# Kernel tuning notes

Hardware: AMD Instinct MI355X
Metric: run time of the kernel (lower is better)

The kernel has to match this reference:

```python
import jax, jax.numpy as jnp
import numpy as np

EMBED_DIM = 1024
NUM_HEADS = 16
HEAD_DIM = EMBED_DIM // NUM_HEADS


def setup_inputs() -> dict:
    key = jax.random.key(0)
    ks = jax.random.split(key, 5)
    x = jax.random.normal(ks[0], (2, 2048, EMBED_DIM), dtype=jnp.float32)
    s_in = 1.0 / np.sqrt(EMBED_DIM)
    W_qkv = jax.random.uniform(ks[1], (EMBED_DIM, 3 * EMBED_DIM), minval=-s_in, maxval=s_in, dtype=jnp.float32)
    b_qkv = jax.random.uniform(ks[2], (3 * EMBED_DIM,), minval=-s_in, maxval=s_in, dtype=jnp.float32)
    W_out = jax.random.uniform(ks[3], (EMBED_DIM, EMBED_DIM), minval=-s_in, maxval=s_in, dtype=jnp.float32)
    b_out = jax.random.uniform(ks[4], (EMBED_DIM,), minval=-s_in, maxval=s_in, dtype=jnp.float32)
    return {"x": x, "W_qkv": W_qkv, "b_qkv": b_qkv, "W_out": W_out, "b_out": b_out}


def reference(x, W_qkv, b_qkv, W_out, b_out):
    B, S, D = x.shape
    H, Dh = NUM_HEADS, HEAD_DIM
    qkv = x @ W_qkv + b_qkv                       # [B, S, 3D]
    q, k, v = jnp.split(qkv, 3, axis=-1)
    # [B, S, D] -> [B, H, S, Dh]
    q = q.reshape(B, S, H, Dh).transpose(0, 2, 1, 3)
    k = k.reshape(B, S, H, Dh).transpose(0, 2, 1, 3)
    v = v.reshape(B, S, H, Dh).transpose(0, 2, 1, 3)
    scores = jnp.einsum('bhqd,bhkd->bhqk', q, k) / jnp.sqrt(jnp.float32(Dh))
    probs = jax.nn.softmax(scores, axis=-1)       # [B, H, S, S]
    attn = jnp.einsum('bhqk,bhkd->bhqd', probs, v)
    attn = attn.transpose(0, 2, 1, 3).reshape(B, S, D)
    return attn @ W_out + b_out
```

## Files before the change

### kernel.cpp

```cpp
#include <hip/hip_runtime.h>
#include <hip/hip_bf16.h>

#define DEV __device__ __forceinline__

typedef __bf16 bf16x8 __attribute__((ext_vector_type(8)));
typedef float f32x4 __attribute__((ext_vector_type(4)));
typedef float f32x16 __attribute__((ext_vector_type(16)));
using u16 = unsigned short;
using u32 = unsigned int;

static constexpr int S = 2048;
static constexpr int D = 1024;
static constexpr float SCQ = 0.125f * 1.44269504088896340736f;

DEV u16 f2bf(float f) {
  unsigned u = __builtin_bit_cast(unsigned, f);
  u += 0x7fffu + ((u >> 16) & 1u);
  return (u16)(u >> 16);
}
DEV u32 pk2(float a, float b) {
  u32 ua = __builtin_bit_cast(u32, a) + 0x8000u;
  u32 ub = __builtin_bit_cast(u32, b) + 0x8000u;
  return __builtin_amdgcn_perm(ub, ua, 0x07060302);
}

__global__ void k_pack(const float* __restrict__ in, u16* __restrict__ out, int n4) {
  int i = blockIdx.x * blockDim.x + threadIdx.x;
  if (i < n4) {
    const float4 v = reinterpret_cast<const float4*>(in)[i];
    ushort4 o;
    o.x = f2bf(v.x); o.y = f2bf(v.y); o.z = f2bf(v.z); o.w = f2bf(v.w);
    reinterpret_cast<ushort4*>(out)[i] = o;
  }
}

__global__ void k_transpose(const float* __restrict__ in, u16* __restrict__ out, int R, int C) {
  __shared__ float t[32][33];
  int c0 = blockIdx.x * 32, r0 = blockIdx.y * 32;
  for (int i = threadIdx.y; i < 32; i += 8)
    t[i][threadIdx.x] = in[(size_t)(r0 + i) * C + c0 + threadIdx.x];
  __syncthreads();
  for (int i = threadIdx.y; i < 32; i += 8)
    out[(size_t)(c0 + i) * R + r0 + threadIdx.x] = f2bf(t[threadIdx.x][i]);
}

template <int MODE>
__global__ __launch_bounds__(256) void k_gemm(const u16* __restrict__ A, const u16* __restrict__ Bt,
                                              const float* __restrict__ bias, int M, int N, int K,
                                              u16* __restrict__ Qb, u16* __restrict__ Kb,
                                              u16* __restrict__ Vt, float* __restrict__ outF) {
  __shared__ u16 As[128][40];
  __shared__ u16 Bs[128][40];
  const int tid = threadIdx.x;
  const int lane = tid & 63, wave = tid >> 6;
  const int l15 = lane & 15, quad = lane >> 4;
  const int m0 = blockIdx.y * 128, n0 = blockIdx.x * 128;
  const int wm = (wave >> 1) * 64, wn = (wave & 1) * 64;
  const int row0 = tid >> 2, c0 = (tid & 3) * 8;
  const int row1 = (tid + 256) >> 2, c1 = (tid & 3) * 8;

  f32x4 acc[4][4];
#pragma unroll
  for (int i = 0; i < 4; i++)
#pragma unroll
    for (int j = 0; j < 4; j++) acc[i][j] = (f32x4){0.f, 0.f, 0.f, 0.f};

  uint4 pa0 = *reinterpret_cast<const uint4*>(&A[(size_t)(m0 + row0) * K + c0]);
  uint4 pa1 = *reinterpret_cast<const uint4*>(&A[(size_t)(m0 + row1) * K + c1]);
  uint4 pb0 = *reinterpret_cast<const uint4*>(&Bt[(size_t)(n0 + row0) * K + c0]);
  uint4 pb1 = *reinterpret_cast<const uint4*>(&Bt[(size_t)(n0 + row1) * K + c1]);

  for (int kk = 0; kk < K; kk += 32) {
    __syncthreads();
    *reinterpret_cast<uint4*>(&As[row0][c0]) = pa0;
    *reinterpret_cast<uint4*>(&As[row1][c1]) = pa1;
    *reinterpret_cast<uint4*>(&Bs[row0][c0]) = pb0;
    *reinterpret_cast<uint4*>(&Bs[row1][c1]) = pb1;
    __syncthreads();
    if (kk + 32 < K) {
      pa0 = *reinterpret_cast<const uint4*>(&A[(size_t)(m0 + row0) * K + kk + 32 + c0]);
      pa1 = *reinterpret_cast<const uint4*>(&A[(size_t)(m0 + row1) * K + kk + 32 + c1]);
      pb0 = *reinterpret_cast<const uint4*>(&Bt[(size_t)(n0 + row0) * K + kk + 32 + c0]);
      pb1 = *reinterpret_cast<const uint4*>(&Bt[(size_t)(n0 + row1) * K + kk + 32 + c1]);
    }
    bf16x8 af[4], bfv[4];
#pragma unroll
    for (int i = 0; i < 4; i++) {
      af[i] = *reinterpret_cast<const bf16x8*>(&As[wm + i * 16 + l15][quad * 8]);
      bfv[i] = *reinterpret_cast<const bf16x8*>(&Bs[wn + i * 16 + l15][quad * 8]);
    }
#pragma unroll
    for (int i = 0; i < 4; i++)
#pragma unroll
      for (int j = 0; j < 4; j++)
        acc[i][j] = __builtin_amdgcn_mfma_f32_16x16x32_bf16(af[i], bfv[j], acc[i][j], 0, 0, 0);
  }

#pragma unroll
  for (int i = 0; i < 4; i++) {
#pragma unroll
    for (int j = 0; j < 4; j++) {
#pragma unroll
      for (int r = 0; r < 4; r++) {
        int m = m0 + wm + i * 16 + quad * 4 + r;
        int n = n0 + wn + j * 16 + l15;
        float v = acc[i][j][r] + bias[n];
        if (MODE == 0) {
          int which = n >> 10;
          int h = (n >> 6) & 15, dh = n & 63;
          int b = m >> 11, s = m & 2047;
          int bh = b * 16 + h;
          if (which == 0)      Qb[((size_t)bh * S + s) * 64 + dh] = f2bf(v * SCQ);
          else if (which == 1) Kb[((size_t)bh * S + s) * 64 + dh] = f2bf(v);
          else                 Vt[((size_t)bh * 64 + dh) * S + s] = f2bf(v);
        } else {
          outF[(size_t)m * N + n] = v;
        }
      }
    }
  }
}

__global__ __launch_bounds__(256, 2) void k_attn(const u16* __restrict__ Qb,
                                                 const u16* __restrict__ Kb,
                                                 const u16* __restrict__ Vt,
                                                 u16* __restrict__ attnB) {
  __shared__ u16 Ks[64][72];
  __shared__ u16 Vs[64][72];
  __shared__ u16 Pl[4][32][72];
  const int bh = blockIdx.y;
  const int q0 = blockIdx.x * 128;
  const int tid = threadIdx.x;
  const int lane = tid & 63, wave = tid >> 6;
  const int l31 = lane & 31, hi = lane >> 5;
  const u16* Qh = Qb + (size_t)bh * S * 64;
  const u16* Kh = Kb + (size_t)bh * S * 64;
  const u16* Vh = Vt + (size_t)bh * 64 * S;
  const int qrow = q0 + wave * 32 + l31;
  bf16x8 qf[4];
#pragma unroll
  for (int f = 0; f < 4; f++)
    qf[f] = *reinterpret_cast<const bf16x8*>(&Qh[(size_t)qrow * 64 + f * 16 + hi * 8]);

  const int r0 = tid >> 3, c0 = (tid & 7) * 8;

  float li = 0.f;
  f32x16 o0, o1;
#pragma unroll
  for (int r = 0; r < 16; r++) { o0[r] = 0.f; o1[r] = 0.f; }

  uint4 pk0 = *reinterpret_cast<const uint4*>(&Kh[(size_t)r0 * 64 + c0]);
  uint4 pk1 = *reinterpret_cast<const uint4*>(&Kh[(size_t)(r0 + 32) * 64 + c0]);
  uint4 pv0 = *reinterpret_cast<const uint4*>(&Vh[(size_t)r0 * S + c0]);
  uint4 pv1 = *reinterpret_cast<const uint4*>(&Vh[(size_t)(r0 + 32) * S + c0]);

  for (int kb = 0; kb < S / 64; kb++) {
    __syncthreads();
    *reinterpret_cast<uint4*>(&Ks[r0][c0]) = pk0;
    *reinterpret_cast<uint4*>(&Ks[r0 + 32][c0]) = pk1;
    *reinterpret_cast<uint4*>(&Vs[r0][c0]) = pv0;
    *reinterpret_cast<uint4*>(&Vs[r0 + 32][c0]) = pv1;
    __syncthreads();
    if (kb + 1 < S / 64) {
      const u16* Kn = Kh + (size_t)(kb + 1) * 64 * 64;
      pk0 = *reinterpret_cast<const uint4*>(&Kn[(size_t)r0 * 64 + c0]);
      pk1 = *reinterpret_cast<const uint4*>(&Kn[(size_t)(r0 + 32) * 64 + c0]);
      pv0 = *reinterpret_cast<const uint4*>(&Vh[(size_t)r0 * S + (kb + 1) * 64 + c0]);
      pv1 = *reinterpret_cast<const uint4*>(&Vh[(size_t)(r0 + 32) * S + (kb + 1) * 64 + c0]);
    }
    f32x16 z[2];
#pragma unroll
    for (int kt = 0; kt < 2; kt++) {
#pragma unroll
      for (int r = 0; r < 16; r++) z[kt][r] = 0.f;
#pragma unroll
      for (int f = 0; f < 4; f++) {
        const bf16x8 a = *reinterpret_cast<const bf16x8*>(&Ks[kt * 32 + l31][f * 16 + hi * 8]);
        z[kt] = __builtin_amdgcn_mfma_f32_32x32x16_bf16(a, qf[f], z[kt], 0, 0, 0);
      }
    }
    float s0 = 0.f, s1 = 0.f, s2 = 0.f, s3 = 0.f;
#pragma unroll
    for (int kt = 0; kt < 2; kt++)
#pragma unroll
      for (int r = 0; r < 16; r++) {
        const float p = __builtin_amdgcn_exp2f(z[kt][r]);
        z[kt][r] = p;
        if ((r & 3) == 0) s0 += p; else if ((r & 3) == 1) s1 += p;
        else if ((r & 3) == 2) s2 += p; else s3 += p;
      }
    li += (s0 + s1) + (s2 + s3);
#pragma unroll
    for (int kt = 0; kt < 2; kt++)
#pragma unroll
      for (int g = 0; g < 4; g++) {
        uint2 pw;
        pw.x = pk2(z[kt][g * 4 + 0], z[kt][g * 4 + 1]);
        pw.y = pk2(z[kt][g * 4 + 2], z[kt][g * 4 + 3]);
        *reinterpret_cast<uint2*>(&Pl[wave][l31][kt * 32 + g * 8 + hi * 4]) = pw;
      }
#pragma unroll
    for (int f = 0; f < 4; f++) {
      const bf16x8 bp = *reinterpret_cast<const bf16x8*>(&Pl[wave][l31][f * 16 + hi * 8]);
      const bf16x8 av0 = *reinterpret_cast<const bf16x8*>(&Vs[l31][f * 16 + hi * 8]);
      const bf16x8 av1 = *reinterpret_cast<const bf16x8*>(&Vs[32 + l31][f * 16 + hi * 8]);
      o0 = __builtin_amdgcn_mfma_f32_32x32x16_bf16(av0, bp, o0, 0, 0, 0);
      o1 = __builtin_amdgcn_mfma_f32_32x32x16_bf16(av1, bp, o1, 0, 0, 0);
    }
  }
  li += __shfl_xor(li, 32);
  const float inv = 1.f / li;
#pragma unroll
  for (int dt = 0; dt < 2; dt++) {
    const f32x16& od = dt ? o1 : o0;
#pragma unroll
    for (int g = 0; g < 4; g++) {
      uint2 ow;
      ow.x = pk2(od[g * 4 + 0] * inv, od[g * 4 + 1] * inv);
      ow.y = pk2(od[g * 4 + 2] * inv, od[g * 4 + 3] * inv);
      *reinterpret_cast<uint2*>(&Pl[wave][l31][dt * 32 + g * 8 + hi * 4]) = ow;
    }
  }
  const int b = bh >> 4, h = bh & 15;
  const int mbase = b * S + q0 + wave * 32;
  const int qr = lane >> 1, ch = (lane & 1) * 32;
  u16* dst = &attnB[(size_t)(mbase + qr) * D + h * 64 + ch];
#pragma unroll
  for (int c = 0; c < 4; c++)
    reinterpret_cast<uint4*>(dst)[c] = *reinterpret_cast<const uint4*>(&Pl[wave][qr][ch + c * 8]);
}

extern "C" void kernel_launch(void* const* d_in, const int* in_sizes, int n_in,
                              void* d_out, int out_size, void* d_ws, size_t ws_size,
                              hipStream_t stream) {
  const float* x = (const float*)d_in[0];
  const float* Wqkv = (const float*)d_in[1];
  const float* bqkv = (const float*)d_in[2];
  const float* Wout = (const float*)d_in[3];
  const float* bout = (const float*)d_in[4];
  float* out = (float*)d_out;

  char* p = (char*)d_ws;
  u16* Xb = (u16*)p;    p += (size_t)4096 * 1024 * 2;
  u16* WqkvT = (u16*)p; p += (size_t)3072 * 1024 * 2;
  u16* WoutT = (u16*)p; p += (size_t)1024 * 1024 * 2;
  u16* Qb = (u16*)p;    p += (size_t)32 * 2048 * 64 * 2;
  u16* Kb = (u16*)p;    p += (size_t)32 * 2048 * 64 * 2;
  u16* Vt = (u16*)p;    p += (size_t)32 * 64 * 2048 * 2;
  u16* attnB = (u16*)p; p += (size_t)4096 * 1024 * 2;

  k_pack<<<4096, 256, 0, stream>>>(x, Xb, 4096 * 1024 / 4);
  k_transpose<<<dim3(3072 / 32, 1024 / 32), dim3(32, 8), 0, stream>>>(Wqkv, WqkvT, 1024, 3072);
  k_transpose<<<dim3(1024 / 32, 1024 / 32), dim3(32, 8), 0, stream>>>(Wout, WoutT, 1024, 1024);
  k_gemm<0><<<dim3(3072 / 128, 4096 / 128), 256, 0, stream>>>(Xb, WqkvT, bqkv, 4096, 3072, 1024,
                                                              Qb, Kb, Vt, nullptr);
  k_attn<<<dim3(2048 / 128, 32), 256, 0, stream>>>(Qb, Kb, Vt, attnB);
  k_gemm<1><<<dim3(1024 / 128, 4096 / 128), 256, 0, stream>>>(attnB, WoutT, bout, 4096, 1024, 1024,
                                                              nullptr, nullptr, nullptr, out);
}
```

Before: 202.4 us.

## Merge prep kernels, stage V transpose through LDS, narrow output GEMM tile

Fuses the x pack and both weight transposes into one launch to cut launch overhead. The QKV GEMM epilogue now stages V tiles in shared memory so the transposed Vt writes become coalesced 16-byte stores, and Q/K use a cheaper rounding conversion. The output projection GEMM uses a 128x64 tile, doubling its grid to fill more CUs. It adds extra LDS use and barriers in the V epilogue, and the simpler rounding differs slightly from round-to-nearest-even.

```diff
diff --git a/kernel.cpp b/kernel.cpp
--- a/kernel.cpp
+++ b/kernel.cpp
@@ -18,106 +18,166 @@
   u += 0x7fffu + ((u >> 16) & 1u);
   return (u16)(u >> 16);
 }
+DEV u16 f2bfr(float f) {
+  return (u16)((__builtin_bit_cast(u32, f) + 0x8000u) >> 16);
+}
 DEV u32 pk2(float a, float b) {
   u32 ua = __builtin_bit_cast(u32, a) + 0x8000u;
   u32 ub = __builtin_bit_cast(u32, b) + 0x8000u;
   return __builtin_amdgcn_perm(ub, ua, 0x07060302);
 }
 
-__global__ void k_pack(const float* __restrict__ in, u16* __restrict__ out, int n4) {
-  int i = blockIdx.x * blockDim.x + threadIdx.x;
-  if (i < n4) {
-    const float4 v = reinterpret_cast<const float4*>(in)[i];
+__global__ __launch_bounds__(256) void k_prep(const float* __restrict__ x, u16* __restrict__ Xb,
+                                              const float* __restrict__ Wqkv, u16* __restrict__ WqkvT,
+                                              const float* __restrict__ Wout, u16* __restrict__ WoutT) {
+  __shared__ float t[32][33];
+  const int bid = blockIdx.x;
+  const int tid = threadIdx.x;
+  if (bid < 4096) {
+    const int i = bid * 256 + tid;
+    const float4 v = reinterpret_cast<const float4*>(x)[i];
     ushort4 o;
     o.x = f2bf(v.x); o.y = f2bf(v.y); o.z = f2bf(v.z); o.w = f2bf(v.w);
-    reinterpret_cast<ushort4*>(out)[i] = o;
-  }
-}
-
-__global__ void k_transpose(const float* __restrict__ in, u16* __restrict__ out, int R, int C) {
-  __shared__ float t[32][33];
-  int c0 = blockIdx.x * 32, r0 = blockIdx.y * 32;
-  for (int i = threadIdx.y; i < 32; i += 8)
-    t[i][threadIdx.x] = in[(size_t)(r0 + i) * C + c0 + threadIdx.x];
+    reinterpret_cast<ushort4*>(Xb)[i] = o;
+    return;
+  }
+  const float* in;
+  u16* out;
+  int R, C, bx, by;
+  if (bid < 4096 + 3072) {
+    const int b = bid - 4096;
+    in = Wqkv; out = WqkvT; R = 1024; C = 3072;
+    bx = b % 96; by = b / 96;
+  } else {
+    const int b = bid - 7168;
+    in = Wout; out = WoutT; R = 1024; C = 1024;
+    bx = b & 31; by = b >> 5;
+  }
+  const int tx = tid & 31, ty = tid >> 5;
+  const int c0 = bx * 32, r0 = by * 32;
+  for (int i = ty; i < 32; i += 8)
+    t[i][tx] = in[(size_t)(r0 + i) * C + c0 + tx];
   __syncthreads();
-  for (int i = threadIdx.y; i < 32; i += 8)
-    out[(size_t)(c0 + i) * R + r0 + threadIdx.x] = f2bf(t[threadIdx.x][i]);
-}
-
-template <int MODE>
+  for (int i = ty; i < 32; i += 8)
+    out[(size_t)(c0 + i) * R + r0 + tx] = f2bf(t[tx][i]);
+}
+
+template <int MODE, int TN>
 __global__ __launch_bounds__(256) void k_gemm(const u16* __restrict__ A, const u16* __restrict__ Bt,
                                               const float* __restrict__ bias, int M, int N, int K,
                                               u16* __restrict__ Qb, u16* __restrict__ Kb,
                                               u16* __restrict__ Vt, float* __restrict__ outF) {
+  constexpr int NJ = TN / 32;
   __shared__ u16 As[128][40];
-  __shared__ u16 Bs[128][40];
+  __shared__ u16 Bs[TN][40];
   const int tid = threadIdx.x;
   const int lane = tid & 63, wave = tid >> 6;
   const int l15 = lane & 15, quad = lane >> 4;
-  const int m0 = blockIdx.y * 128, n0 = blockIdx.x * 128;
-  const int wm = (wave >> 1) * 64, wn = (wave & 1) * 64;
+  const int m0 = blockIdx.y * 128, n0 = blockIdx.x * TN;
+  const int wm = (wave >> 1) * 64, wn = (wave & 1) * (TN / 2);
   const int row0 = tid >> 2, c0 = (tid & 3) * 8;
-  const int row1 = (tid + 256) >> 2, c1 = (tid & 3) * 8;
-
-  f32x4 acc[4][4];
+  const int row1 = row0 + 64;
+
+  f32x4 acc[4][NJ];
 #pragma unroll
   for (int i = 0; i < 4; i++)
 #pragma unroll
-    for (int j = 0; j < 4; j++) acc[i][j] = (f32x4){0.f, 0.f, 0.f, 0.f};
+    for (int j = 0; j < NJ; j++) acc[i][j] = (f32x4){0.f, 0.f, 0.f, 0.f};
 
   uint4 pa0 = *reinterpret_cast<const uint4*>(&A[(size_t)(m0 + row0) * K + c0]);
-  uint4 pa1 = *reinterpret_cast<const uint4*>(&A[(size_t)(m0 + row1) * K + c1]);
+  uint4 pa1 = *reinterpret_cast<const uint4*>(&A[(size_t)(m0 + row1) * K + c0]);
   uint4 pb0 = *reinterpret_cast<const uint4*>(&Bt[(size_t)(n0 + row0) * K + c0]);
-  uint4 pb1 = *reinterpret_cast<const uint4*>(&Bt[(size_t)(n0 + row1) * K + c1]);
+  uint4 pb1;
+  if constexpr (TN == 128) pb1 = *reinterpret_cast<const uint4*>(&Bt[(size_t)(n0 + row1) * K + c0]);
 
   for (int kk = 0; kk < K; kk += 32) {
     __syncthreads();
     *reinterpret_cast<uint4*>(&As[row0][c0]) = pa0;
-    *reinterpret_cast<uint4*>(&As[row1][c1]) = pa1;
-    *reinterpret_cast<uint4*>(&Bs[row0][c0]) = pb0;
-    *reinterpret_cast<uint4*>(&Bs[row1][c1]) = pb1;
+    *reinterpret_cast<uint4*>(&As[row1][c0]) = pa1;
+    *reinterpret_cast<uint4*>(&Bs[row0 & (TN - 1)][c0]) = pb0;
+    if constexpr (TN == 128) *reinterpret_cast<uint4*>(&Bs[row1][c0]) = pb1;
     __syncthreads();
     if (kk + 32 < K) {
       pa0 = *reinterpret_cast<const uint4*>(&A[(size_t)(m0 + row0) * K + kk + 32 + c0]);
-      pa1 = *reinterpret_cast<const uint4*>(&A[(size_t)(m0 + row1) * K + kk + 32 + c1]);
+      pa1 = *reinterpret_cast<const uint4*>(&A[(size_t)(m0 + row1) * K + kk + 32 + c0]);
       pb0 = *reinterpret_cast<const uint4*>(&Bt[(size_t)(n0 + row0) * K + kk + 32 + c0]);
-      pb1 = *reinterpret_cast<const uint4*>(&Bt[(size_t)(n0 + row1) * K + kk + 32 + c1]);
-    }
-    bf16x8 af[4], bfv[4];
-#pragma unroll
-    for (int i = 0; i < 4; i++) {
+      if constexpr (TN == 128)
+        pb1 = *reinterpret_cast<const uint4*>(&Bt[(size_t)(n0 + row1) * K + kk + 32 + c0]);
+    }
+    bf16x8 af[4], bfv[NJ];
+#pragma unroll
+    for (int i = 0; i < 4; i++)
       af[i] = *reinterpret_cast<const bf16x8*>(&As[wm + i * 16 + l15][quad * 8]);
-      bfv[i] = *reinterpret_cast<const bf16x8*>(&Bs[wn + i * 16 + l15][quad * 8]);
-    }
+#pragma unroll
+    for (int j = 0; j < NJ; j++)
+      bfv[j] = *reinterpret_cast<const bf16x8*>(&Bs[wn + j * 16 + l15][quad * 8]);
 #pragma unroll
     for (int i = 0; i < 4; i++)
 #pragma unroll
-      for (int j = 0; j < 4; j++)
+      for (int j = 0; j < NJ; j++)
         acc[i][j] = __builtin_amdgcn_mfma_f32_16x16x32_bf16(af[i], bfv[j], acc[i][j], 0, 0, 0);
   }
 
-#pragma unroll
-  for (int i = 0; i < 4; i++) {
-#pragma unroll
-    for (int j = 0; j < 4; j++) {
-#pragma unroll
-      for (int r = 0; r < 4; r++) {
-        int m = m0 + wm + i * 16 + quad * 4 + r;
-        int n = n0 + wn + j * 16 + l15;
-        float v = acc[i][j][r] + bias[n];
-        if (MODE == 0) {
-          int which = n >> 10;
-          int h = (n >> 6) & 15, dh = n & 63;
-          int b = m >> 11, s = m & 2047;
-          int bh = b * 16 + h;
-          if (which == 0)      Qb[((size_t)bh * S + s) * 64 + dh] = f2bf(v * SCQ);
-          else if (which == 1) Kb[((size_t)bh * S + s) * 64 + dh] = f2bf(v);
-          else                 Vt[((size_t)bh * 64 + dh) * S + s] = f2bf(v);
-        } else {
-          outF[(size_t)m * N + n] = v;
+  if constexpr (MODE == 0) {
+    __shared__ u16 LT[64][136];
+    if (n0 >= 2048) {
+      const int b = m0 >> 11, sbase = m0 & 2047;
+#pragma unroll
+      for (int p = 0; p < 2; p++) {
+        __syncthreads();
+        if ((wave & 1) == p) {
+#pragma unroll
+          for (int j = 0; j < NJ; j++) {
+            const int n = n0 + wn + j * 16 + l15;
+            const float vb = bias[n];
+#pragma unroll
+            for (int i = 0; i < 4; i++) {
+              uint2 pw;
+              pw.x = pk2(acc[i][j][0] + vb, acc[i][j][1] + vb);
+              pw.y = pk2(acc[i][j][2] + vb, acc[i][j][3] + vb);
+              *reinterpret_cast<uint2*>(&LT[j * 16 + l15][wm + i * 16 + quad * 4]) = pw;
+            }
+          }
         }
-      }
-    }
+        __syncthreads();
+        const int h = ((n0 - 2048) >> 6) + p;
+        const int bh = b * 16 + h;
+        const int nl = tid >> 2, cc = (tid & 3) * 32;
+        u16* dst = &Vt[((size_t)bh * 64 + nl) * S + sbase + cc];
+#pragma unroll
+        for (int k = 0; k < 4; k++)
+          reinterpret_cast<uint4*>(dst)[k] = *reinterpret_cast<const uint4*>(&LT[nl][cc + k * 8]);
+      }
+    } else {
+#pragma unroll
+      for (int i = 0; i < 4; i++) {
+#pragma unroll
+        for (int j = 0; j < NJ; j++) {
+#pragma unroll
+          for (int r = 0; r < 4; r++) {
+            const int m = m0 + wm + i * 16 + quad * 4 + r;
+            const int n = n0 + wn + j * 16 + l15;
+            const float v = acc[i][j][r] + bias[n];
+            const int h = (n >> 6) & 15, dh = n & 63;
+            const int b = m >> 11, s = m & 2047;
+            const int bh = b * 16 + h;
+            if (n < 1024) Qb[((size_t)bh * S + s) * 64 + dh] = f2bfr(v * SCQ);
+            else          Kb[((size_t)bh * S + s) * 64 + dh] = f2bfr(v);
+          }
+        }
+      }
+    }
+  } else {
+#pragma unroll
+    for (int i = 0; i < 4; i++)
+#pragma unroll
+      for (int j = 0; j < NJ; j++)
+#pragma unroll
+        for (int r = 0; r < 4; r++) {
+          const int m = m0 + wm + i * 16 + quad * 4 + r;
+          const int n = n0 + wn + j * 16 + l15;
+          outF[(size_t)m * N + n] = acc[i][j][r] + bias[n];
+        }
   }
 }
 
@@ -249,12 +309,10 @@
   u16* Vt = (u16*)p;    p += (size_t)32 * 64 * 2048 * 2;
   u16* attnB = (u16*)p; p += (size_t)4096 * 1024 * 2;
 
-  k_pack<<<4096, 256, 0, stream>>>(x, Xb, 4096 * 1024 / 4);
-  k_transpose<<<dim3(3072 / 32, 1024 / 32), dim3(32, 8), 0, stream>>>(Wqkv, WqkvT, 1024, 3072);
-  k_transpose<<<dim3(1024 / 32, 1024 / 32), dim3(32, 8), 0, stream>>>(Wout, WoutT, 1024, 1024);
-  k_gemm<0><<<dim3(3072 / 128, 4096 / 128), 256, 0, stream>>>(Xb, WqkvT, bqkv, 4096, 3072, 1024,
-                                                              Qb, Kb, Vt, nullptr);
+  k_prep<<<4096 + 3072 + 1024, 256, 0, stream>>>(x, Xb, Wqkv, WqkvT, Wout, WoutT);
+  k_gemm<0, 128><<<dim3(3072 / 128, 4096 / 128), 256, 0, stream>>>(
+      Xb, WqkvT, bqkv, 4096, 3072, 1024, Qb, Kb, Vt, nullptr);
   k_attn<<<dim3(2048 / 128, 32), 256, 0, stream>>>(Qb, Kb, Vt, attnB);
-  k_gemm<1><<<dim3(1024 / 128, 4096 / 128), 256, 0, stream>>>(attnB, WoutT, bout, 4096, 1024, 1024,
-                                                              nullptr, nullptr, nullptr, out);
-}
+  k_gemm<1, 64><<<dim3(1024 / 64, 4096 / 128), 256, 0, stream>>>(
+      attnB, WoutT, bout, 4096, 1024, 1024, nullptr, nullptr, nullptr, out);
+}
```

New measurement: 200.6 us, median of 2. About the same (-0.9%).
